# Kernel optimization log

Hardware: AMD Instinct MI355X
Metric: run time of the kernel (lower is better)

## Reference

```python
import jax, jax.numpy as jnp
import numpy as np

B, S, D, H, DH = 2, 2048, 768, 12, 64
GAMMA = 0.5
SMOOTHING = 1.0  # softmax_attn_smoothing scalar (non-trainable weight in the original)
SCALE = 1.0 / float(np.sqrt(DH))


def setup_inputs() -> dict:
    key = jax.random.key(0)
    ks = jax.random.split(key, 8)
    w = 0.02
    return {
        "inp": jax.random.normal(ks[0], (B, S, D), dtype=jnp.float32),
        "pos_emb": jax.random.normal(ks[1], (S, D), dtype=jnp.float32),
        "Wq_inp": jax.random.normal(ks[2], (D, H * DH), dtype=jnp.float32) * w,
        "Wk_inp": jax.random.normal(ks[3], (D, H * DH), dtype=jnp.float32) * w,
        "Wq_pos": jax.random.normal(ks[4], (D, H * DH), dtype=jnp.float32) * w,
        "Wk_pos": jax.random.normal(ks[5], (D, H * DH), dtype=jnp.float32) * w,
        "Wv": jax.random.normal(ks[6], (D, H * DH), dtype=jnp.float32) * w,
        "Wo": jax.random.normal(ks[7], (H * DH, D), dtype=jnp.float32) * w,
    }


def reference(inp, pos_emb, Wq_inp, Wk_inp, Wq_pos, Wk_pos, Wv, Wo):
    # projections; note original reshape order: [..., d_head, n_head]
    q_i = (inp @ Wq_inp).reshape(B, S, DH, H)
    k_i = (inp @ Wk_inp).reshape(B, S, DH, H)
    q_p = (pos_emb @ Wq_pos).reshape(S, DH, H)
    k_p = (pos_emb @ Wk_pos).reshape(S, DH, H)
    v = (inp @ Wv).reshape(B, S, DH, H)

    # content-content stream: [B,S,S,H], softmax over key axis (axis=2)
    score_inp = jnp.einsum("bidh,bjdh->bijh", q_i, k_i) * (SCALE * SMOOTHING)
    prob_inp = jax.nn.softmax(score_inp, axis=2)

    # position-position stream: [S,S,H], softmax over key axis (axis=1)
    score_pos = jnp.einsum("idh,jdh->ijh", q_p, k_p) * (SCALE * SMOOTHING)
    prob_pos = jax.nn.softmax(score_pos, axis=1)[None]  # [1,S,S,H]

    # gamma blend of the two attention distributions
    attn_prob = (1.0 - GAMMA) * prob_inp + GAMMA * prob_pos  # [B,S,S,H]

    # V-weighted sum, merge heads as [..., h, d] per the original 'bihd' output
    attn_out = jnp.einsum("bijh,bjdh->bihd", attn_prob, v).reshape(B, S, H * DH)
    attn_out = attn_out @ Wo  # [B,S,D]
    return attn_out, attn_prob
```

## Files before the change

### kernel.cpp

```cpp
#include <hip/hip_runtime.h>
#include <hip/hip_bf16.h>

constexpr int NH  = 12;
constexpr int SEQ = 2048;
constexpr int DHD = 64;
constexpr int DIM = 768;
constexpr float QSCALE = 0.125f * 1.44269504088896f;

typedef __bf16 bf16x8 __attribute__((ext_vector_type(8)));
typedef __bf16 bf16x4 __attribute__((ext_vector_type(4)));
typedef float  f32x4  __attribute__((ext_vector_type(4)));

#define MFMA16(a, b, c) __builtin_amdgcn_mfma_f32_16x16x32_bf16((a), (b), (c), 0, 0, 0)

__global__ __launch_bounds__(256) void conv_kernel(
    const float* __restrict__ inp, const float* __restrict__ pos,
    __bf16* __restrict__ Ab, __bf16* __restrict__ Pb)
{
    const int idx = blockIdx.x * 256 + threadIdx.x;
    constexpr int N8I = 4096 * 768 / 8;
    constexpr int N8P = 2048 * 768 / 8;
    if (idx >= N8I + N8P) return;
    const float* src; __bf16* dst; int off;
    if (idx < N8I) { src = inp; dst = Ab; off = idx; }
    else           { src = pos; dst = Pb; off = idx - N8I; }
    const float4 v0 = *reinterpret_cast<const float4*>(&src[(size_t)off * 8]);
    const float4 v1 = *reinterpret_cast<const float4*>(&src[(size_t)off * 8 + 4]);
    bf16x8 t;
    t[0] = (__bf16)v0.x; t[1] = (__bf16)v0.y; t[2] = (__bf16)v0.z; t[3] = (__bf16)v0.w;
    t[4] = (__bf16)v1.x; t[5] = (__bf16)v1.y; t[6] = (__bf16)v1.z; t[7] = (__bf16)v1.w;
    *reinterpret_cast<bf16x8*>(&dst[(size_t)off * 8]) = t;
}

__global__ __launch_bounds__(256) void packw_kernel(
    const float* __restrict__ Wqi, const float* __restrict__ Wki,
    const float* __restrict__ Wvv, const float* __restrict__ Wqp,
    const float* __restrict__ Wkp, __bf16* __restrict__ Wp)
{
    const int kt = blockIdx.x, h = blockIdx.y, z = blockIdx.z;
    const int k0 = kt * 64;
    const float* W; float scale = 1.0f;
    if (z == 0)      { W = Wqi; scale = QSCALE; }
    else if (z == 1) { W = Wki; }
    else if (z == 2) { W = Wvv; }
    else if (z == 3) { W = Wqp; scale = QSCALE; }
    else             { W = Wkp; }

    __shared__ __bf16 lds[64][68];
    const int tid = threadIdx.x;
    {
        const int d = tid & 63, kq = tid >> 6;
        #pragma unroll
        for (int rep = 0; rep < 16; ++rep) {
            const int kk = rep * 4 + kq;
            lds[kk][d] = (__bf16)(W[(size_t)(k0 + kk) * DIM + d * 12 + h] * scale);
        }
    }
    __syncthreads();
    {
        const int k = tid & 63, dq = tid >> 6;
        const size_t slab = ((size_t)z * 12 + h) * 64;
        #pragma unroll
        for (int rep = 0; rep < 16; ++rep) {
            const int d = rep * 4 + dq;
            Wp[(slab + d) * DIM + k0 + k] = lds[k][d];
        }
    }
}

__global__ __launch_bounds__(256) void proj_kernel(
    const __bf16* __restrict__ Ab, const __bf16* __restrict__ Pb,
    const __bf16* __restrict__ Wp,
    __bf16* __restrict__ Qi, __bf16* __restrict__ Ki, __bf16* __restrict__ Vsd,
    __bf16* __restrict__ Qp, __bf16* __restrict__ Kp)
{
    const int bx = blockIdx.x, h = blockIdx.y, z = blockIdx.z;
    if (z >= 3 && bx >= 8) return;
    const int tid = threadIdx.x, lane = tid & 63, wv = tid >> 6;
    const int l15 = lane & 15, lg = lane >> 4;
    const int m_w = bx * 256 + wv * 64;

    const __bf16* Asrc = (z < 3) ? Ab : Pb;
    const __bf16* Wsl = Wp + ((size_t)z * 12 + h) * 64 * DIM;

    f32x4 acc[4][4] = {};

    for (int kt = 0; kt < 24; ++kt) {
        const int k0 = kt * 32;
        bf16x8 a[4], b[4];
        #pragma unroll
        for (int mf = 0; mf < 4; ++mf)
            a[mf] = *reinterpret_cast<const bf16x8*>(
                &Asrc[(size_t)(m_w + mf * 16 + l15) * DIM + k0 + lg * 8]);
        #pragma unroll
        for (int nf = 0; nf < 4; ++nf)
            b[nf] = *reinterpret_cast<const bf16x8*>(
                &Wsl[(size_t)(nf * 16 + l15) * DIM + k0 + lg * 8]);
        #pragma unroll
        for (int mf = 0; mf < 4; ++mf)
            #pragma unroll
            for (int nf = 0; nf < 4; ++nf)
                acc[mf][nf] = MFMA16(a[mf], b[nf], acc[mf][nf]);
    }

    __bf16* outp = (z == 0) ? Qi : (z == 1) ? Ki : (z == 2) ? Vsd : (z == 3) ? Qp : Kp;
    #pragma unroll
    for (int mf = 0; mf < 4; ++mf)
        #pragma unroll
        for (int r = 0; r < 4; ++r) {
            const int m = m_w + mf * 16 + lg * 4 + r;
            const int s = m & 2047;
            const int slab = (z < 3) ? ((m >> 11) * 12 + h) : h;
            const size_t base = ((size_t)slab * SEQ + s) * DHD;
            #pragma unroll
            for (int nf = 0; nf < 4; ++nf)
                outp[base + nf * 16 + l15] = (__bf16)acc[mf][nf][r];
        }
}

__global__ __launch_bounds__(256) void vtrans_kernel(
    const __bf16* __restrict__ Vsd, __bf16* __restrict__ Vt)
{
    const int s0 = blockIdx.x * 64, slab = blockIdx.y;
    __shared__ __bf16 lds[64][66];
    const int tid = threadIdx.x;
    {
        const int rr = tid >> 3, cq = tid & 7;
        #pragma unroll
        for (int rep = 0; rep < 2; ++rep) {
            const int r2 = rr + rep * 32;
            *reinterpret_cast<bf16x8*>(&lds[r2][cq * 8]) =
                *reinterpret_cast<const bf16x8*>(
                    &Vsd[((size_t)slab * SEQ + s0 + r2) * DHD + cq * 8]);
        }
    }
    __syncthreads();
    {
        const int dd = tid >> 3, sq = tid & 7;
        #pragma unroll
        for (int rep = 0; rep < 2; ++rep) {
            const int d2 = dd + rep * 32;
            bf16x8 v;
            #pragma unroll
            for (int q = 0; q < 8; ++q) v[q] = lds[sq * 8 + q][d2];
            *reinterpret_cast<bf16x8*>(&Vt[((size_t)slab * DHD + d2) * SEQ + s0 + sq * 8]) = v;
        }
    }
}

__global__ __launch_bounds__(256) void pv_kernel(
    const __bf16* __restrict__ Qi, const __bf16* __restrict__ Ki,
    const __bf16* __restrict__ Qp, const __bf16* __restrict__ Kp,
    const __bf16* __restrict__ Vt,
    float* __restrict__ l_ws, float* __restrict__ attn_pre)
{
    const int itb = blockIdx.x, slab = blockIdx.y;
    const int b = slab / 12, h = slab - b * 12;
    const int tid = threadIdx.x, lane = tid & 63, wv = tid >> 6;
    const int l15 = lane & 15, lg = lane >> 4;
    const int i0 = itb * 64 + wv * 16;

    const __bf16* Qib = Qi + (((size_t)b * NH + h) * SEQ + i0) * DHD;
    const __bf16* Qpb = Qp + ((size_t)h * SEQ + i0) * DHD;
    const __bf16* Kib = Ki + ((size_t)b * NH + h) * SEQ * DHD;
    const __bf16* Kpb = Kp + (size_t)h * SEQ * DHD;
    const __bf16* Vtb = Vt + ((size_t)b * NH + h) * DHD * SEQ;

    bf16x8 aQi[2], aQp[2];
    #pragma unroll
    for (int ks = 0; ks < 2; ++ks) {
        aQi[ks] = *reinterpret_cast<const bf16x8*>(
            &Qib[(size_t)l15 * DHD + ks * 32 + lg * 8]);
        aQp[ks] = *reinterpret_cast<const bf16x8*>(
            &Qpb[(size_t)l15 * DHD + ks * 32 + lg * 8]);
    }

    __shared__ __align__(16) __bf16 ppv[2][4][2][16][36];
    f32x4 acc_i[4] = {}, acc_p[4] = {};
    float li[4] = {}, lp[4] = {};

    #pragma unroll 2
    for (int jt = 0; jt < 64; ++jt) {
        const int j0 = jt * 32;
        const int par = jt & 1;

        f32x4 ci[2] = {}, cq[2] = {};
        #pragma unroll
        for (int ks = 0; ks < 2; ++ks)
            #pragma unroll
            for (int nf = 0; nf < 2; ++nf) {
                const bf16x8 bi_ = *reinterpret_cast<const bf16x8*>(
                    &Kib[(size_t)(j0 + nf * 16 + l15) * DHD + ks * 32 + lg * 8]);
                const bf16x8 bp_ = *reinterpret_cast<const bf16x8*>(
                    &Kpb[(size_t)(j0 + nf * 16 + l15) * DHD + ks * 32 + lg * 8]);
                ci[nf] = MFMA16(aQi[ks], bi_, ci[nf]);
                cq[nf] = MFMA16(aQp[ks], bp_, cq[nf]);
            }

        #pragma unroll
        for (int r = 0; r < 4; ++r) {
            const int i = lg * 4 + r;
            #pragma unroll
            for (int nf = 0; nf < 2; ++nf) {
                const float pi_ = exp2f(ci[nf][r]);
                const float pq_ = exp2f(cq[nf][r]);
                li[r] += pi_;
                lp[r] += pq_;
                ppv[par][wv][0][i][nf * 16 + l15] = (__bf16)pi_;
                ppv[par][wv][1][i][nf * 16 + l15] = (__bf16)pq_;
            }
        }

        const bf16x8 api = *reinterpret_cast<const bf16x8*>(&ppv[par][wv][0][l15][lg * 8]);
        const bf16x8 app = *reinterpret_cast<const bf16x8*>(&ppv[par][wv][1][l15][lg * 8]);
        #pragma unroll
        for (int nf = 0; nf < 4; ++nf) {
            const bf16x8 bv = *reinterpret_cast<const bf16x8*>(
                &Vtb[(size_t)(nf * 16 + l15) * SEQ + j0 + lg * 8]);
            acc_i[nf] = MFMA16(api, bv, acc_i[nf]);
            acc_p[nf] = MFMA16(app, bv, acc_p[nf]);
        }
    }

    #pragma unroll
    for (int msk = 1; msk < 16; msk <<= 1)
        #pragma unroll
        for (int r = 0; r < 4; ++r) {
            li[r] += __shfl_xor(li[r], msk);
            lp[r] += __shfl_xor(lp[r], msk);
        }

    if (l15 == 0) {
        #pragma unroll
        for (int r = 0; r < 4; ++r) {
            const int i = i0 + lg * 4 + r;
            l_ws[((size_t)b * NH + h) * SEQ + i] = li[r];
            l_ws[((size_t)2 * NH + h) * SEQ + i] = lp[r];
        }
    }

    #pragma unroll
    for (int nf = 0; nf < 4; ++nf)
        #pragma unroll
        for (int r = 0; r < 4; ++r) {
            const int i = i0 + lg * 4 + r;
            attn_pre[((size_t)(b * SEQ + i)) * DIM + h * DHD + nf * 16 + l15] =
                0.5f * (acc_i[nf][r] / li[r] + acc_p[nf][r] / lp[r]);
        }
}

__global__ __launch_bounds__(256) void emit_kernel(
    const __bf16* __restrict__ Qi, const __bf16* __restrict__ Ki,
    const __bf16* __restrict__ Qp, const __bf16* __restrict__ Kp,
    const float* __restrict__ l_ws, float* __restrict__ out1)
{
    const int bid = blockIdx.x;
    const int wg = (bid & 7) * 128 + (bid >> 3);
    const int it = wg & 127, jsg = (wg >> 7) & 3, b = wg >> 9;

    const int i0 = it * 16;
    const int tid = threadIdx.x, lane = tid & 63, wv = tid >> 6;
    const int l15 = lane & 15, lg = lane >> 4;
    const int js = jsg * 4 + wv;

    __shared__ __align__(16) __bf16 pbuf[4][16][32][12];
    __shared__ float ml[12][16][2];

    if (tid < 192) {
        const int h = tid >> 4, i = tid & 15;
        ml[h][i][0] = 0.5f / l_ws[((size_t)b * NH + h) * SEQ + i0 + i];
        ml[h][i][1] = 0.5f / l_ws[((size_t)2 * NH + h) * SEQ + i0 + i];
    }
    __syncthreads();

    const __bf16* pf = &pbuf[wv][0][0][0];

    #pragma unroll 1
    for (int jt = 0; jt < 4; ++jt) {
        const int j0 = js * 128 + jt * 32;

        #pragma unroll 2
        for (int h = 0; h < 12; ++h) {
            const __bf16* Qib = Qi + (((size_t)b * NH + h) * SEQ + i0) * DHD;
            const __bf16* Qpb = Qp + ((size_t)h * SEQ + i0) * DHD;
            const __bf16* Kib = Ki + ((size_t)b * NH + h) * SEQ * DHD;
            const __bf16* Kpb = Kp + (size_t)h * SEQ * DHD;

            f32x4 ci[2] = {}, cq[2] = {};
            #pragma unroll
            for (int ks = 0; ks < 2; ++ks) {
                const bf16x8 aQi = *reinterpret_cast<const bf16x8*>(
                    &Qib[(size_t)l15 * DHD + ks * 32 + lg * 8]);
                const bf16x8 aQp = *reinterpret_cast<const bf16x8*>(
                    &Qpb[(size_t)l15 * DHD + ks * 32 + lg * 8]);
                #pragma unroll
                for (int nf = 0; nf < 2; ++nf) {
                    const bf16x8 bi_ = *reinterpret_cast<const bf16x8*>(
                        &Kib[(size_t)(j0 + nf * 16 + l15) * DHD + ks * 32 + lg * 8]);
                    const bf16x8 bp_ = *reinterpret_cast<const bf16x8*>(
                        &Kpb[(size_t)(j0 + nf * 16 + l15) * DHD + ks * 32 + lg * 8]);
                    ci[nf] = MFMA16(aQi, bi_, ci[nf]);
                    cq[nf] = MFMA16(aQp, bp_, cq[nf]);
                }
            }

            #pragma unroll
            for (int r = 0; r < 4; ++r) {
                const int i = lg * 4 + r;
                const float s0 = ml[h][i][0], s1 = ml[h][i][1];
                #pragma unroll
                for (int nf = 0; nf < 2; ++nf) {
                    const float pi_ = exp2f(ci[nf][r]) * s0;
                    const float pq_ = exp2f(cq[nf][r]) * s1;
                    pbuf[wv][i][nf * 16 + l15][h] = (__bf16)(pi_ + pq_);
                }
            }
        }

        #pragma unroll
        for (int k = 0; k < 24; ++k) {
            const int o = k * 256 + 4 * lane;
            const int i = o / 384;
            const int rem = o - i * 384;
            const bf16x4 pv4 = *reinterpret_cast<const bf16x4*>(&pf[o]);
            f32x4 v;
            #pragma unroll
            for (int q = 0; q < 4; ++q) v[q] = (float)pv4[q];
            const size_t addr = ((size_t)(b * SEQ + i0 + i) * SEQ + j0) * 12 + rem;
            *reinterpret_cast<f32x4*>(&out1[addr]) = v;
        }
    }
}

__global__ __launch_bounds__(256) void final_kernel(
    const float* __restrict__ A, const float* __restrict__ W, float* __restrict__ out0)
{
    const int m0 = blockIdx.y * 64;
    const int n0 = blockIdx.x * 192;

    __shared__ __bf16 Al[64][32];
    __shared__ __bf16 Wl[192][32];

    const int tid = threadIdx.x;
    const int lane = tid & 63, wv = tid >> 6;
    const int wm = wv >> 1, wn = wv & 1;
    const int l15 = lane & 15, lg = lane >> 4;

    f32x4 c[2][6] = {};

    for (int kt = 0; kt < 24; ++kt) {
        const int k0 = kt * 32;
        __syncthreads();
        {
            const int r = tid >> 3, kq = tid & 7;
            #pragma unroll
            for (int rep = 0; rep < 2; ++rep) {
                const float4 v = *reinterpret_cast<const float4*>(
                    &A[(size_t)(m0 + r + rep * 32) * DIM + k0 + kq * 4]);
                bf16x4 t;
                t[0] = (__bf16)v.x; t[1] = (__bf16)v.y; t[2] = (__bf16)v.z; t[3] = (__bf16)v.w;
                *reinterpret_cast<bf16x4*>(&Al[r + rep * 32][kq * 4]) = t;
            }
        }
        for (int idx = tid; idx < 32 * 48; idx += 256) {
            const int k = idx / 48, nq = idx - k * 48;
            const float4 v = *reinterpret_cast<const float4*>(
                &W[(size_t)(k0 + k) * DIM + n0 + nq * 4]);
            Wl[nq * 4 + 0][k] = (__bf16)v.x;
            Wl[nq * 4 + 1][k] = (__bf16)v.y;
            Wl[nq * 4 + 2][k] = (__bf16)v.z;
            Wl[nq * 4 + 3][k] = (__bf16)v.w;
        }
        __syncthreads();

        bf16x8 a[2], b[6];
        #pragma unroll
        for (int mf = 0; mf < 2; ++mf)
            a[mf] = *reinterpret_cast<const bf16x8*>(&Al[wm * 32 + mf * 16 + l15][lg * 8]);
        #pragma unroll
        for (int nf = 0; nf < 6; ++nf)
            b[nf] = *reinterpret_cast<const bf16x8*>(&Wl[wn * 96 + nf * 16 + l15][lg * 8]);
        #pragma unroll
        for (int mf = 0; mf < 2; ++mf)
            #pragma unroll
            for (int nf = 0; nf < 6; ++nf)
                c[mf][nf] = MFMA16(a[mf], b[nf], c[mf][nf]);
    }

    #pragma unroll
    for (int mf = 0; mf < 2; ++mf)
        #pragma unroll
        for (int nf = 0; nf < 6; ++nf)
            #pragma unroll
            for (int r = 0; r < 4; ++r) {
                const int m = m0 + wm * 32 + mf * 16 + lg * 4 + r;
                const int n = n0 + wn * 96 + nf * 16 + l15;
                out0[(size_t)m * DIM + n] = c[mf][nf][r];
            }
}

extern "C" void kernel_launch(void* const* d_in, const int* in_sizes, int n_in,
                              void* d_out, int out_size, void* d_ws, size_t ws_size,
                              hipStream_t stream)
{
    (void)in_sizes; (void)n_in; (void)out_size; (void)ws_size;

    const float* inp = (const float*)d_in[0];
    const float* pos = (const float*)d_in[1];
    const float* Wqi = (const float*)d_in[2];
    const float* Wki = (const float*)d_in[3];
    const float* Wqp = (const float*)d_in[4];
    const float* Wkp = (const float*)d_in[5];
    const float* Wvv = (const float*)d_in[6];
    const float* Wo  = (const float*)d_in[7];

    char* w = (char*)d_ws;
    __bf16* Ab = (__bf16*)w;  w += (size_t)4096 * 768 * 2;
    __bf16* Pb = (__bf16*)w;  w += (size_t)2048 * 768 * 2;
    __bf16* Wp = (__bf16*)w;  w += (size_t)5 * 768 * 768 * 2;
    __bf16* Qi = (__bf16*)w;  w += (size_t)2 * NH * SEQ * DHD * 2;
    __bf16* Ki = (__bf16*)w;  w += (size_t)2 * NH * SEQ * DHD * 2;
    __bf16* Vsd = (__bf16*)w; w += (size_t)2 * NH * SEQ * DHD * 2;
    __bf16* Qp = (__bf16*)w;  w += (size_t)NH * SEQ * DHD * 2;
    __bf16* Kp = (__bf16*)w;  w += (size_t)NH * SEQ * DHD * 2;
    float* l_ws = (float*)w;  w += (size_t)3 * NH * SEQ * 4;
    float* attn_pre = (float*)w; w += (size_t)4096 * DIM * 4;
    __bf16* Vt = Ab;

    float* out0 = (float*)d_out;
    float* out1 = out0 + (size_t)2 * SEQ * DIM;

    hipLaunchKernelGGL(conv_kernel, dim3(2304), dim3(256), 0, stream, inp, pos, Ab, Pb);
    hipLaunchKernelGGL(packw_kernel, dim3(12, 12, 5), dim3(256), 0, stream,
                       Wqi, Wki, Wvv, Wqp, Wkp, Wp);
    hipLaunchKernelGGL(proj_kernel, dim3(16, 12, 5), dim3(256), 0, stream,
                       Ab, Pb, Wp, Qi, Ki, Vsd, Qp, Kp);
    hipLaunchKernelGGL(vtrans_kernel, dim3(32, 24), dim3(256), 0, stream, Vsd, Vt);
    hipLaunchKernelGGL(pv_kernel, dim3(32, 24), dim3(256), 0, stream,
                       Qi, Ki, Qp, Kp, Vt, l_ws, attn_pre);
    hipLaunchKernelGGL(emit_kernel, dim3(1024), dim3(256), 0, stream,
                       Qi, Ki, Qp, Kp, l_ws, out1);
    hipLaunchKernelGGL(final_kernel, dim3(4, 64, 1), dim3(256), 0, stream,
                       attn_pre, Wo, out0);
}
```

Measured before the change: 758.8 us.

## Split PV kernel into content and batch-shared position passes

```diff
diff --git a/kernel.cpp b/kernel.cpp
--- a/kernel.cpp
+++ b/kernel.cpp
@@ -148,11 +148,10 @@
     }
 }
 
-__global__ __launch_bounds__(256) void pv_kernel(
+__global__ __launch_bounds__(256) void pv_c_kernel(
     const __bf16* __restrict__ Qi, const __bf16* __restrict__ Ki,
-    const __bf16* __restrict__ Qp, const __bf16* __restrict__ Kp,
     const __bf16* __restrict__ Vt,
-    float* __restrict__ l_ws, float* __restrict__ attn_pre)
+    float* __restrict__ l_ws, float* __restrict__ Oi)
 {
     const int itb = blockIdx.x, slab = blockIdx.y;
     const int b = slab / 12, h = slab - b * 12;
@@ -161,40 +160,32 @@
     const int i0 = itb * 64 + wv * 16;
 
     const __bf16* Qib = Qi + (((size_t)b * NH + h) * SEQ + i0) * DHD;
-    const __bf16* Qpb = Qp + ((size_t)h * SEQ + i0) * DHD;
     const __bf16* Kib = Ki + ((size_t)b * NH + h) * SEQ * DHD;
-    const __bf16* Kpb = Kp + (size_t)h * SEQ * DHD;
     const __bf16* Vtb = Vt + ((size_t)b * NH + h) * DHD * SEQ;
 
-    bf16x8 aQi[2], aQp[2];
-    #pragma unroll
-    for (int ks = 0; ks < 2; ++ks) {
-        aQi[ks] = *reinterpret_cast<const bf16x8*>(
+    bf16x8 aQ[2];
+    #pragma unroll
+    for (int ks = 0; ks < 2; ++ks)
+        aQ[ks] = *reinterpret_cast<const bf16x8*>(
             &Qib[(size_t)l15 * DHD + ks * 32 + lg * 8]);
-        aQp[ks] = *reinterpret_cast<const bf16x8*>(
-            &Qpb[(size_t)l15 * DHD + ks * 32 + lg * 8]);
-    }
-
-    __shared__ __align__(16) __bf16 ppv[2][4][2][16][36];
-    f32x4 acc_i[4] = {}, acc_p[4] = {};
-    float li[4] = {}, lp[4] = {};
+
+    __shared__ __align__(16) __bf16 ppv[2][4][16][36];
+    f32x4 acc[4] = {};
+    float li[4] = {};
 
     #pragma unroll 2
     for (int jt = 0; jt < 64; ++jt) {
         const int j0 = jt * 32;
         const int par = jt & 1;
 
-        f32x4 ci[2] = {}, cq[2] = {};
+        f32x4 ci[2] = {};
         #pragma unroll
         for (int ks = 0; ks < 2; ++ks)
             #pragma unroll
             for (int nf = 0; nf < 2; ++nf) {
                 const bf16x8 bi_ = *reinterpret_cast<const bf16x8*>(
                     &Kib[(size_t)(j0 + nf * 16 + l15) * DHD + ks * 32 + lg * 8]);
-                const bf16x8 bp_ = *reinterpret_cast<const bf16x8*>(
-                    &Kpb[(size_t)(j0 + nf * 16 + l15) * DHD + ks * 32 + lg * 8]);
-                ci[nf] = MFMA16(aQi[ks], bi_, ci[nf]);
-                cq[nf] = MFMA16(aQp[ks], bp_, cq[nf]);
+                ci[nf] = MFMA16(aQ[ks], bi_, ci[nf]);
             }
 
         #pragma unroll
@@ -202,41 +193,116 @@
             const int i = lg * 4 + r;
             #pragma unroll
             for (int nf = 0; nf < 2; ++nf) {
-                const float pi_ = exp2f(ci[nf][r]);
-                const float pq_ = exp2f(cq[nf][r]);
-                li[r] += pi_;
-                lp[r] += pq_;
-                ppv[par][wv][0][i][nf * 16 + l15] = (__bf16)pi_;
-                ppv[par][wv][1][i][nf * 16 + l15] = (__bf16)pq_;
-            }
-        }
-
-        const bf16x8 api = *reinterpret_cast<const bf16x8*>(&ppv[par][wv][0][l15][lg * 8]);
-        const bf16x8 app = *reinterpret_cast<const bf16x8*>(&ppv[par][wv][1][l15][lg * 8]);
+                const float p = exp2f(ci[nf][r]);
+                li[r] += p;
+                ppv[par][wv][i][nf * 16 + l15] = (__bf16)p;
+            }
+        }
+
+        const bf16x8 ap = *reinterpret_cast<const bf16x8*>(&ppv[par][wv][l15][lg * 8]);
         #pragma unroll
         for (int nf = 0; nf < 4; ++nf) {
             const bf16x8 bv = *reinterpret_cast<const bf16x8*>(
                 &Vtb[(size_t)(nf * 16 + l15) * SEQ + j0 + lg * 8]);
-            acc_i[nf] = MFMA16(api, bv, acc_i[nf]);
-            acc_p[nf] = MFMA16(app, bv, acc_p[nf]);
+            acc[nf] = MFMA16(ap, bv, acc[nf]);
         }
     }
 
     #pragma unroll
     for (int msk = 1; msk < 16; msk <<= 1)
         #pragma unroll
-        for (int r = 0; r < 4; ++r) {
+        for (int r = 0; r < 4; ++r)
             li[r] += __shfl_xor(li[r], msk);
-            lp[r] += __shfl_xor(lp[r], msk);
-        }
 
     if (l15 == 0) {
+        #pragma unroll
+        for (int r = 0; r < 4; ++r)
+            l_ws[((size_t)b * NH + h) * SEQ + i0 + lg * 4 + r] = li[r];
+    }
+
+    #pragma unroll
+    for (int nf = 0; nf < 4; ++nf)
         #pragma unroll
         for (int r = 0; r < 4; ++r) {
             const int i = i0 + lg * 4 + r;
-            l_ws[((size_t)b * NH + h) * SEQ + i] = li[r];
-            l_ws[((size_t)2 * NH + h) * SEQ + i] = lp[r];
-        }
+            Oi[((size_t)(b * SEQ + i)) * DIM + h * DHD + nf * 16 + l15] =
+                0.5f * acc[nf][r] / li[r];
+        }
+}
+
+__global__ __launch_bounds__(256) void pv_p_kernel(
+    const __bf16* __restrict__ Qp, const __bf16* __restrict__ Kp,
+    const __bf16* __restrict__ Vt,
+    float* __restrict__ l_ws, float* __restrict__ Op)
+{
+    const int itb = blockIdx.x, h = blockIdx.y;
+    const int tid = threadIdx.x, lane = tid & 63, wv = tid >> 6;
+    const int l15 = lane & 15, lg = lane >> 4;
+    const int i0 = itb * 64 + wv * 16;
+
+    const __bf16* Qpb = Qp + ((size_t)h * SEQ + i0) * DHD;
+    const __bf16* Kpb = Kp + (size_t)h * SEQ * DHD;
+    const __bf16* Vt0 = Vt + ((size_t)0 * NH + h) * DHD * SEQ;
+    const __bf16* Vt1 = Vt + ((size_t)1 * NH + h) * DHD * SEQ;
+
+    bf16x8 aQ[2];
+    #pragma unroll
+    for (int ks = 0; ks < 2; ++ks)
+        aQ[ks] = *reinterpret_cast<const bf16x8*>(
+            &Qpb[(size_t)l15 * DHD + ks * 32 + lg * 8]);
+
+    __shared__ __align__(16) __bf16 ppv[2][4][16][36];
+    f32x4 acc0[4] = {}, acc1[4] = {};
+    float lp[4] = {};
+
+    #pragma unroll 2
+    for (int jt = 0; jt < 64; ++jt) {
+        const int j0 = jt * 32;
+        const int par = jt & 1;
+
+        f32x4 cq[2] = {};
+        #pragma unroll
+        for (int ks = 0; ks < 2; ++ks)
+            #pragma unroll
+            for (int nf = 0; nf < 2; ++nf) {
+                const bf16x8 bp_ = *reinterpret_cast<const bf16x8*>(
+                    &Kpb[(size_t)(j0 + nf * 16 + l15) * DHD + ks * 32 + lg * 8]);
+                cq[nf] = MFMA16(aQ[ks], bp_, cq[nf]);
+            }
+
+        #pragma unroll
+        for (int r = 0; r < 4; ++r) {
+            const int i = lg * 4 + r;
+            #pragma unroll
+            for (int nf = 0; nf < 2; ++nf) {
+                const float p = exp2f(cq[nf][r]);
+                lp[r] += p;
+                ppv[par][wv][i][nf * 16 + l15] = (__bf16)p;
+            }
+        }
+
+        const bf16x8 ap = *reinterpret_cast<const bf16x8*>(&ppv[par][wv][l15][lg * 8]);
+        #pragma unroll
+        for (int nf = 0; nf < 4; ++nf) {
+            const bf16x8 bv0 = *reinterpret_cast<const bf16x8*>(
+                &Vt0[(size_t)(nf * 16 + l15) * SEQ + j0 + lg * 8]);
+            const bf16x8 bv1 = *reinterpret_cast<const bf16x8*>(
+                &Vt1[(size_t)(nf * 16 + l15) * SEQ + j0 + lg * 8]);
+            acc0[nf] = MFMA16(ap, bv0, acc0[nf]);
+            acc1[nf] = MFMA16(ap, bv1, acc1[nf]);
+        }
+    }
+
+    #pragma unroll
+    for (int msk = 1; msk < 16; msk <<= 1)
+        #pragma unroll
+        for (int r = 0; r < 4; ++r)
+            lp[r] += __shfl_xor(lp[r], msk);
+
+    if (l15 == 0) {
+        #pragma unroll
+        for (int r = 0; r < 4; ++r)
+            l_ws[((size_t)2 * NH + h) * SEQ + i0 + lg * 4 + r] = lp[r];
     }
 
     #pragma unroll
@@ -244,8 +310,9 @@
         #pragma unroll
         for (int r = 0; r < 4; ++r) {
             const int i = i0 + lg * 4 + r;
-            attn_pre[((size_t)(b * SEQ + i)) * DIM + h * DHD + nf * 16 + l15] =
-                0.5f * (acc_i[nf][r] / li[r] + acc_p[nf][r] / lp[r]);
+            const float inv = 0.5f / lp[r];
+            Op[((size_t)(0 * SEQ + i)) * DIM + h * DHD + nf * 16 + l15] = acc0[nf][r] * inv;
+            Op[((size_t)(1 * SEQ + i)) * DIM + h * DHD + nf * 16 + l15] = acc1[nf][r] * inv;
         }
 }
 
@@ -279,7 +346,7 @@
     for (int jt = 0; jt < 4; ++jt) {
         const int j0 = js * 128 + jt * 32;
 
-        #pragma unroll 2
+        #pragma unroll 1
         for (int h = 0; h < 12; ++h) {
             const __bf16* Qib = Qi + (((size_t)b * NH + h) * SEQ + i0) * DHD;
             const __bf16* Qpb = Qp + ((size_t)h * SEQ + i0) * DHD;
@@ -333,7 +400,8 @@
 }
 
 __global__ __launch_bounds__(256) void final_kernel(
-    const float* __restrict__ A, const float* __restrict__ W, float* __restrict__ out0)
+    const float* __restrict__ Oi, const float* __restrict__ Op,
+    const float* __restrict__ W, float* __restrict__ out0)
 {
     const int m0 = blockIdx.y * 64;
     const int n0 = blockIdx.x * 192;
@@ -355,10 +423,12 @@
             const int r = tid >> 3, kq = tid & 7;
             #pragma unroll
             for (int rep = 0; rep < 2; ++rep) {
-                const float4 v = *reinterpret_cast<const float4*>(
-                    &A[(size_t)(m0 + r + rep * 32) * DIM + k0 + kq * 4]);
+                const size_t base = (size_t)(m0 + r + rep * 32) * DIM + k0 + kq * 4;
+                const float4 vi = *reinterpret_cast<const float4*>(&Oi[base]);
+                const float4 vp = *reinterpret_cast<const float4*>(&Op[base]);
                 bf16x4 t;
-                t[0] = (__bf16)v.x; t[1] = (__bf16)v.y; t[2] = (__bf16)v.z; t[3] = (__bf16)v.w;
+                t[0] = (__bf16)(vi.x + vp.x); t[1] = (__bf16)(vi.y + vp.y);
+                t[2] = (__bf16)(vi.z + vp.z); t[3] = (__bf16)(vi.w + vp.w);
                 *reinterpret_cast<bf16x4*>(&Al[r + rep * 32][kq * 4]) = t;
             }
         }
@@ -424,7 +494,8 @@
     __bf16* Qp = (__bf16*)w;  w += (size_t)NH * SEQ * DHD * 2;
     __bf16* Kp = (__bf16*)w;  w += (size_t)NH * SEQ * DHD * 2;
     float* l_ws = (float*)w;  w += (size_t)3 * NH * SEQ * 4;
-    float* attn_pre = (float*)w; w += (size_t)4096 * DIM * 4;
+    float* Oi = (float*)w;    w += (size_t)4096 * DIM * 4;
+    float* Op = (float*)w;    w += (size_t)4096 * DIM * 4;
     __bf16* Vt = Ab;
 
     float* out0 = (float*)d_out;
@@ -436,10 +507,12 @@
     hipLaunchKernelGGL(proj_kernel, dim3(16, 12, 5), dim3(256), 0, stream,
                        Ab, Pb, Wp, Qi, Ki, Vsd, Qp, Kp);
     hipLaunchKernelGGL(vtrans_kernel, dim3(32, 24), dim3(256), 0, stream, Vsd, Vt);
-    hipLaunchKernelGGL(pv_kernel, dim3(32, 24), dim3(256), 0, stream,
-                       Qi, Ki, Qp, Kp, Vt, l_ws, attn_pre);
+    hipLaunchKernelGGL(pv_c_kernel, dim3(32, 24), dim3(256), 0, stream,
+                       Qi, Ki, Vt, l_ws, Oi);
+    hipLaunchKernelGGL(pv_p_kernel, dim3(32, 12), dim3(256), 0, stream,
+                       Qp, Kp, Vt, l_ws, Op);
     hipLaunchKernelGGL(emit_kernel, dim3(1024), dim3(256), 0, stream,
                        Qi, Ki, Qp, Kp, l_ws, out1);
     hipLaunchKernelGGL(final_kernel, dim3(4, 64, 1), dim3(256), 0, stream,
-                       attn_pre, Wo, out0);
-}
+                       Oi, Op, Wo, out0);
+}
```

Result: slower. 836.2 us (+10.2%).
